# Kernel tuning notes

Hardware: AMD Instinct MI355X
Metric: run time of the kernel (lower is better)

## Reference

```python
import jax, jax.numpy as jnp
import numpy as np

N_NODES = 50000
N_EDGES = 600000
IN_DIM = 16
HIDDEN = 128
OUT_DIM = 4


def _sage_conv(x, src, dst, Wl, Wr, b, n_nodes):
    # PyG SAGEConv (aggr='mean'): out = lin_l(mean_{j in N(i)} x_j) + lin_r(x_i)
    msg = x[src]  # [E, F] gather
    s = jax.ops.segment_sum(msg, dst, num_segments=n_nodes)  # [N, F]
    cnt = jax.ops.segment_sum(jnp.ones((src.shape[0], 1), x.dtype), dst,
                              num_segments=n_nodes)  # [N, 1]
    agg = s / jnp.maximum(cnt, 1.0)
    return agg @ Wl.T + x @ Wr.T + b


def setup_inputs() -> dict:
    key = jax.random.key(0)
    ks = jax.random.split(key, 12)
    def glorot(k, shape):
        lim = np.sqrt(6.0 / (shape[0] + shape[1])).astype(np.float32)
        return jax.random.uniform(k, shape, jnp.float32, -lim, lim)
    x = jax.random.normal(ks[0], (N_NODES, IN_DIM), jnp.float32)
    edge_index = jax.random.randint(ks[1], (2, N_EDGES), 0, N_NODES, jnp.int64)
    return {
        "x": x,
        "edge_index": edge_index,
        "Wl1": glorot(ks[2], (HIDDEN, IN_DIM)),
        "Wr1": glorot(ks[3], (HIDDEN, IN_DIM)),
        "b1": jnp.zeros((HIDDEN,), jnp.float32),
        "Wl2": glorot(ks[4], (HIDDEN, HIDDEN)),
        "Wr2": glorot(ks[5], (HIDDEN, HIDDEN)),
        "b2": jnp.zeros((HIDDEN,), jnp.float32),
        "Wl3": glorot(ks[6], (HIDDEN, HIDDEN)),
        "Wr3": glorot(ks[7], (HIDDEN, HIDDEN)),
        "b3": jnp.zeros((HIDDEN,), jnp.float32),
        "Wh": glorot(ks[8], (OUT_DIM, HIDDEN)),
        "bh": jnp.zeros((OUT_DIM,), jnp.float32),
    }


def reference(x, edge_index, Wl1, Wr1, b1, Wl2, Wr2, b2, Wl3, Wr3, b3, Wh, bh):
    src, dst = edge_index[0], edge_index[1]
    n = x.shape[0]
    # dropout is identity in eval mode
    h = jax.nn.relu(_sage_conv(x, src, dst, Wl1, Wr1, b1, n))
    h = jax.nn.relu(_sage_conv(h, src, dst, Wl2, Wr2, b2, n))
    h = jax.nn.relu(_sage_conv(h, src, dst, Wl3, Wr3, b3, n))
    return h @ Wh.T + bh
```

## Files before the change

### kernel.cpp

```cpp
#include <hip/hip_runtime.h>
#include <hip/hip_bf16.h>


#define DEG_SLOTS 64

typedef unsigned short bf16_t;
typedef unsigned int uint32;
typedef __attribute__((ext_vector_type(8))) short bf16x8;
typedef __attribute__((ext_vector_type(4))) float f32x4;

__device__ __forceinline__ bf16_t f2bf(float f) {
    uint32 u = __float_as_uint(f);
    u += 0x7fff + ((u >> 16) & 1);
    return (bf16_t)(u >> 16);
}
__device__ __forceinline__ float bf2f(bf16_t b) {
    return __uint_as_float((uint32)b << 16);
}
__device__ __forceinline__ void acc8(float* acc, uint4 v) {
    acc[0] += bf2f((bf16_t)(v.x & 0xffff)); acc[1] += bf2f((bf16_t)(v.x >> 16));
    acc[2] += bf2f((bf16_t)(v.y & 0xffff)); acc[3] += bf2f((bf16_t)(v.y >> 16));
    acc[4] += bf2f((bf16_t)(v.z & 0xffff)); acc[5] += bf2f((bf16_t)(v.z >> 16));
    acc[6] += bf2f((bf16_t)(v.w & 0xffff)); acc[7] += bf2f((bf16_t)(v.w >> 16));
}

__global__ __launch_bounds__(256) void fill_padded_kernel(
    const int* __restrict__ src, const int* __restrict__ dst,
    int* __restrict__ cnt, int* __restrict__ colp, int E) {
    int i = blockIdx.x * 256 + threadIdx.x;
    int e0 = i * 4;
    if (e0 + 3 < E) {
        int4 s = *(const int4*)&src[e0];
        int4 d = *(const int4*)&dst[e0];
        int p0 = atomicAdd(&cnt[d.x], 1);
        int p1 = atomicAdd(&cnt[d.y], 1);
        int p2 = atomicAdd(&cnt[d.z], 1);
        int p3 = atomicAdd(&cnt[d.w], 1);
        if (p0 < DEG_SLOTS) colp[d.x * DEG_SLOTS + p0] = s.x;
        if (p1 < DEG_SLOTS) colp[d.y * DEG_SLOTS + p1] = s.y;
        if (p2 < DEG_SLOTS) colp[d.z * DEG_SLOTS + p2] = s.z;
        if (p3 < DEG_SLOTS) colp[d.w * DEG_SLOTS + p3] = s.w;
    } else {
        for (int e = e0; e < E; ++e) {
            int d = dst[e];
            int pos = atomicAdd(&cnt[d], 1);
            if (pos < DEG_SLOTS) colp[d * DEG_SLOTS + pos] = src[e];
        }
    }
}

__global__ __launch_bounds__(256) void layer16_fused_kernel(
    const float* __restrict__ x, const int* __restrict__ cnt,
    const int* __restrict__ colp,
    const float* __restrict__ Wl1, const float* __restrict__ Wr1,
    const float* __restrict__ bias, bf16_t* __restrict__ hout, int n) {
    const int t = threadIdx.x;
    const int lane = t & 63;
    const int wave = t >> 6;
    const int r = lane & 15;
    const int q = lane >> 4;
    const int qh = q & 1;
    const int qe = q >> 1;
    const int m0 = blockIdx.x * 32 + (wave >> 1) * 16;
    const int nb = (wave & 1) * 64;

    bf16x8 aF;
    {
        int node = m0 + r;
        if (node >= n) node = n - 1;
        float acc[8];
        #pragma unroll
        for (int j = 0; j < 8; ++j) acc[j] = 0.f;
        const int d = cnt[node];
        const int lo = node * DEG_SLOTS;
        const int hi = lo + d;
        int e = lo + qe;
        int c0 = 0, c1 = 0;
        if (e < hi) c0 = colp[e];
        if (e + 2 < hi) c1 = colp[e + 2];
        for (; e + 2 < hi; e += 4) {
            const int p0 = c0, p1 = c1;
            if (e + 4 < hi) c0 = colp[e + 4];
            if (e + 6 < hi) c1 = colp[e + 6];
            float4 u0 = *(const float4*)&x[p0 * 16 + qh * 8];
            float4 u1 = *(const float4*)&x[p0 * 16 + qh * 8 + 4];
            float4 u2 = *(const float4*)&x[p1 * 16 + qh * 8];
            float4 u3 = *(const float4*)&x[p1 * 16 + qh * 8 + 4];
            acc[0] += u0.x + u2.x; acc[1] += u0.y + u2.y;
            acc[2] += u0.z + u2.z; acc[3] += u0.w + u2.w;
            acc[4] += u1.x + u3.x; acc[5] += u1.y + u3.y;
            acc[6] += u1.z + u3.z; acc[7] += u1.w + u3.w;
        }
        if (e < hi) {
            float4 u0 = *(const float4*)&x[c0 * 16 + qh * 8];
            float4 u1 = *(const float4*)&x[c0 * 16 + qh * 8 + 4];
            acc[0] += u0.x; acc[1] += u0.y; acc[2] += u0.z; acc[3] += u0.w;
            acc[4] += u1.x; acc[5] += u1.y; acc[6] += u1.z; acc[7] += u1.w;
        }
        #pragma unroll
        for (int j = 0; j < 8; ++j) acc[j] += __shfl_xor(acc[j], 32);
        if (q < 2) {
            float iv = 1.0f / (float)max(d, 1);
            #pragma unroll
            for (int j = 0; j < 8; ++j) acc[j] *= iv;
        } else {
            float4 u0 = *(const float4*)&x[node * 16 + qh * 8];
            float4 u1 = *(const float4*)&x[node * 16 + qh * 8 + 4];
            acc[0] = u0.x; acc[1] = u0.y; acc[2] = u0.z; acc[3] = u0.w;
            acc[4] = u1.x; acc[5] = u1.y; acc[6] = u1.z; acc[7] = u1.w;
        }
        #pragma unroll
        for (int j = 0; j < 8; ++j) aF[j] = (short)f2bf(acc[j]);
    }

    #pragma unroll
    for (int nt = 0; nt < 4; ++nt) {
        const int cidx = nb + nt * 16 + r;
        const float* wsrc = (q < 2) ? (Wl1 + cidx * 16 + qh * 8)
                                    : (Wr1 + cidx * 16 + qh * 8);
        float4 w0 = *(const float4*)wsrc;
        float4 w1 = *(const float4*)(wsrc + 4);
        bf16x8 bF;
        bF[0] = (short)f2bf(w0.x); bF[1] = (short)f2bf(w0.y);
        bF[2] = (short)f2bf(w0.z); bF[3] = (short)f2bf(w0.w);
        bF[4] = (short)f2bf(w1.x); bF[5] = (short)f2bf(w1.y);
        bF[6] = (short)f2bf(w1.z); bF[7] = (short)f2bf(w1.w);
        f32x4 acc0 = {0.f, 0.f, 0.f, 0.f};
        acc0 = __builtin_amdgcn_mfma_f32_16x16x32_bf16(aF, bF, acc0, 0, 0, 0);
        float bo = bias[cidx];
        #pragma unroll
        for (int reg = 0; reg < 4; ++reg) {
            int row0 = m0 + q * 4 + reg;
            if (row0 < n)
                hout[(size_t)row0 * 128 + cidx] = f2bf(fmaxf(acc0[reg] + bo, 0.0f));
        }
    }
}

__global__ __launch_bounds__(256) void aggregate128_kernel(
    const bf16_t* __restrict__ h, const int* __restrict__ cnt,
    const int* __restrict__ colp,
    bf16_t* __restrict__ aggb, int N) {
    const int t = threadIdx.x;
    const int node = blockIdx.x * 8 + (t >> 5);
    const int sub = (t >> 4) & 1;
    const int li = t & 15;
    if (node >= N) return;
    const int d = cnt[node];
    const int lo = node * DEG_SLOTS;
    const int hi = lo + d;
    float acc[8];
    #pragma unroll
    for (int j = 0; j < 8; ++j) acc[j] = 0.0f;
    int e = lo + sub;
    int c0 = 0, c1 = 0, c2 = 0, c3 = 0;
    if (e < hi)     c0 = colp[e];
    if (e + 2 < hi) c1 = colp[e + 2];
    if (e + 4 < hi) c2 = colp[e + 4];
    if (e + 6 < hi) c3 = colp[e + 6];
    for (; e + 6 < hi; e += 8) {
        const int s0 = c0, s1 = c1, s2 = c2, s3 = c3;
        if (e + 8  < hi) c0 = colp[e + 8];
        if (e + 10 < hi) c1 = colp[e + 10];
        if (e + 12 < hi) c2 = colp[e + 12];
        if (e + 14 < hi) c3 = colp[e + 14];
        uint4 v0 = *(const uint4*)&h[(size_t)s0 * 128 + li * 8];
        uint4 v1 = *(const uint4*)&h[(size_t)s1 * 128 + li * 8];
        uint4 v2 = *(const uint4*)&h[(size_t)s2 * 128 + li * 8];
        uint4 v3 = *(const uint4*)&h[(size_t)s3 * 128 + li * 8];
        acc8(acc, v0);
        acc8(acc, v1);
        acc8(acc, v2);
        acc8(acc, v3);
    }
    if (e < hi) {
        uint4 v = *(const uint4*)&h[(size_t)c0 * 128 + li * 8];
        acc8(acc, v);
    }
    if (e + 2 < hi) {
        uint4 v = *(const uint4*)&h[(size_t)c1 * 128 + li * 8];
        acc8(acc, v);
    }
    if (e + 4 < hi) {
        uint4 v = *(const uint4*)&h[(size_t)c2 * 128 + li * 8];
        acc8(acc, v);
    }
    #pragma unroll
    for (int j = 0; j < 8; ++j) acc[j] += __shfl_xor(acc[j], 16);
    if (sub == 0) {
        const float iv = 1.0f / (float)max(d, 1);
        uint4 pk;
        pk.x = (uint32)f2bf(acc[0] * iv) | ((uint32)f2bf(acc[1] * iv) << 16);
        pk.y = (uint32)f2bf(acc[2] * iv) | ((uint32)f2bf(acc[3] * iv) << 16);
        pk.z = (uint32)f2bf(acc[4] * iv) | ((uint32)f2bf(acc[5] * iv) << 16);
        pk.w = (uint32)f2bf(acc[6] * iv) | ((uint32)f2bf(acc[7] * iv) << 16);
        *(uint4*)&aggb[(size_t)node * 128 + li * 8] = pk;
    }
}

__global__ __launch_bounds__(256) void layer128_mfma_kernel(
    const bf16_t* __restrict__ aggb, const bf16_t* __restrict__ hin,
    const float* __restrict__ Wl, const float* __restrict__ Wr,
    const float* __restrict__ bias, bf16_t* __restrict__ hout, int n) {
    __shared__ bf16_t w_lds[16384];

    const int t = threadIdx.x;
    const int lane = t & 63;
    const int wave = t >> 6;
    const int r = lane & 15;
    const int q = lane >> 4;
    const int c = blockIdx.x & 1;
    const int rowblk = blockIdx.x >> 1;
    const int nbase = c * 64;
    const int m0w = rowblk * 128 + wave * 32;

    #pragma unroll
    for (int i = 0; i < 8; ++i) {
        int ch  = i * 256 + t;
        int q_  = ch & 3;
        int r_  = (ch >> 2) & 15;
        int ks_ = (ch >> 6) & 7;
        int nt_ = ch >> 9;
        int cidx = nbase + nt_ * 16 + r_;
        int k0 = ks_ * 32 + q_ * 8;
        const float* src = (k0 < 128) ? (Wl + cidx * 128 + k0)
                                      : (Wr + cidx * 128 + (k0 - 128));
        float4 a = *(const float4*)src;
        float4 b = *(const float4*)(src + 4);
        uint4 pk;
        pk.x = (uint32)f2bf(a.x) | ((uint32)f2bf(a.y) << 16);
        pk.y = (uint32)f2bf(a.z) | ((uint32)f2bf(a.w) << 16);
        pk.z = (uint32)f2bf(b.x) | ((uint32)f2bf(b.y) << 16);
        pk.w = (uint32)f2bf(b.z) | ((uint32)f2bf(b.w) << 16);
        *(uint4*)&w_lds[ch * 8] = pk;
    }

    bf16x8 aF[2][8];
    #pragma unroll
    for (int mt = 0; mt < 2; ++mt) {
        int node = m0w + mt * 16 + r;
        if (node >= n) node = n - 1;
        const bf16_t* arow = aggb + (size_t)node * 128;
        const bf16_t* hrow = hin + (size_t)node * 128;
        #pragma unroll
        for (int ks = 0; ks < 4; ++ks)
            aF[mt][ks] = *(const bf16x8*)(arow + ks * 32 + q * 8);
        #pragma unroll
        for (int ks = 0; ks < 4; ++ks)
            aF[mt][4 + ks] = *(const bf16x8*)(hrow + ks * 32 + q * 8);
    }
    __syncthreads();

    #pragma unroll
    for (int nt = 0; nt < 4; ++nt) {
        f32x4 acc0 = {0.f, 0.f, 0.f, 0.f};
        f32x4 acc1 = {0.f, 0.f, 0.f, 0.f};
        #pragma unroll
        for (int ks = 0; ks < 8; ++ks) {
            bf16x8 bF = *(const bf16x8*)&w_lds[(size_t)((nt * 8 + ks) * 64 + r * 4 + q) * 8];
            acc0 = __builtin_amdgcn_mfma_f32_16x16x32_bf16(aF[0][ks], bF, acc0, 0, 0, 0);
            acc1 = __builtin_amdgcn_mfma_f32_16x16x32_bf16(aF[1][ks], bF, acc1, 0, 0, 0);
        }
        const int cidx = nbase + nt * 16 + r;
        const float bo = bias[cidx];
        #pragma unroll
        for (int reg = 0; reg < 4; ++reg) {
            int row0 = m0w + q * 4 + reg;
            if (row0 < n)
                hout[(size_t)row0 * 128 + cidx] = f2bf(fmaxf(acc0[reg] + bo, 0.0f));
            int row1 = m0w + 16 + q * 4 + reg;
            if (row1 < n)
                hout[(size_t)row1 * 128 + cidx] = f2bf(fmaxf(acc1[reg] + bo, 0.0f));
        }
    }
}

__global__ __launch_bounds__(256) void layer128_head_kernel(
    const bf16_t* __restrict__ aggb, const bf16_t* __restrict__ hin,
    const float* __restrict__ Wl, const float* __restrict__ Wr,
    const float* __restrict__ bias, const float* __restrict__ Wh,
    const float* __restrict__ bh, float* __restrict__ out, int n) {
    __shared__ bf16_t w_lds[16384];

    const int t = threadIdx.x;
    const int lane = t & 63;
    const int wave = t >> 6;
    const int r = lane & 15;
    const int q = lane >> 4;
    const int m0w = blockIdx.x * 64 + wave * 16;

    bf16x8 aF[8];
    {
        int node = m0w + r;
        if (node >= n) node = n - 1;
        const bf16_t* arow = aggb + (size_t)node * 128;
        const bf16_t* hrow = hin + (size_t)node * 128;
        #pragma unroll
        for (int ks = 0; ks < 4; ++ks)
            aF[ks] = *(const bf16x8*)(arow + ks * 32 + q * 8);
        #pragma unroll
        for (int ks = 0; ks < 4; ++ks)
            aF[4 + ks] = *(const bf16x8*)(hrow + ks * 32 + q * 8);
    }

    float p[4][4];
    #pragma unroll
    for (int reg = 0; reg < 4; ++reg)
        #pragma unroll
        for (int o = 0; o < 4; ++o) p[reg][o] = 0.f;

    #pragma unroll
    for (int phase = 0; phase < 2; ++phase) {
        if (phase) __syncthreads();
        const int nbase = phase * 64;
        #pragma unroll
        for (int i = 0; i < 8; ++i) {
            int ch  = i * 256 + t;
            int q_  = ch & 3;
            int r_  = (ch >> 2) & 15;
            int ks_ = (ch >> 6) & 7;
            int nt_ = ch >> 9;
            int cidx = nbase + nt_ * 16 + r_;
            int k0 = ks_ * 32 + q_ * 8;
            const float* src = (k0 < 128) ? (Wl + cidx * 128 + k0)
                                          : (Wr + cidx * 128 + (k0 - 128));
            float4 a = *(const float4*)src;
            float4 b = *(const float4*)(src + 4);
            uint4 pk;
            pk.x = (uint32)f2bf(a.x) | ((uint32)f2bf(a.y) << 16);
            pk.y = (uint32)f2bf(a.z) | ((uint32)f2bf(a.w) << 16);
            pk.z = (uint32)f2bf(b.x) | ((uint32)f2bf(b.y) << 16);
            pk.w = (uint32)f2bf(b.z) | ((uint32)f2bf(b.w) << 16);
            *(uint4*)&w_lds[ch * 8] = pk;
        }
        __syncthreads();

        #pragma unroll
        for (int nt = 0; nt < 4; ++nt) {
            f32x4 acc0 = {0.f, 0.f, 0.f, 0.f};
            #pragma unroll
            for (int ks = 0; ks < 8; ++ks) {
                bf16x8 bF = *(const bf16x8*)&w_lds[(size_t)((nt * 8 + ks) * 64 + r * 4 + q) * 8];
                acc0 = __builtin_amdgcn_mfma_f32_16x16x32_bf16(aF[ks], bF, acc0, 0, 0, 0);
            }
            const int cidx = nbase + nt * 16 + r;
            const float bo = bias[cidx];
            const float wh0 = Wh[cidx], wh1 = Wh[128 + cidx];
            const float wh2 = Wh[256 + cidx], wh3 = Wh[384 + cidx];
            #pragma unroll
            for (int reg = 0; reg < 4; ++reg) {
                float h0 = fmaxf(acc0[reg] + bo, 0.0f);
                p[reg][0] += h0 * wh0; p[reg][1] += h0 * wh1;
                p[reg][2] += h0 * wh2; p[reg][3] += h0 * wh3;
            }
        }
    }

    #pragma unroll
    for (int reg = 0; reg < 4; ++reg)
        #pragma unroll
        for (int o = 0; o < 4; ++o) {
            float v = p[reg][o];
            v += __shfl_xor(v, 1);
            v += __shfl_xor(v, 2);
            v += __shfl_xor(v, 4);
            v += __shfl_xor(v, 8);
            if (r == 0) {
                int row = m0w + q * 4 + reg;
                if (row < n) out[(size_t)row * 4 + o] = v + bh[o];
            }
        }
}

extern "C" void kernel_launch(void* const* d_in, const int* in_sizes, int n_in,
                              void* d_out, int out_size, void* d_ws, size_t ws_size,
                              hipStream_t stream) {
    const float* x   = (const float*)d_in[0];
    const int*   ei  = (const int*)d_in[1];
    const float* Wl1 = (const float*)d_in[2];
    const float* Wr1 = (const float*)d_in[3];
    const float* b1  = (const float*)d_in[4];
    const float* Wl2 = (const float*)d_in[5];
    const float* Wr2 = (const float*)d_in[6];
    const float* b2  = (const float*)d_in[7];
    const float* Wl3 = (const float*)d_in[8];
    const float* Wr3 = (const float*)d_in[9];
    const float* b3  = (const float*)d_in[10];
    const float* Wh  = (const float*)d_in[11];
    const float* bh  = (const float*)d_in[12];
    float* out = (float*)d_out;

    const int N = in_sizes[0] / 16;
    const int E = in_sizes[1] / 2;
    const int* src = ei;
    const int* dst = ei + E;

    int* cnt       = (int*)d_ws;
    int* colp      = cnt + ((N + 64) & ~63);
    bf16_t* aggb   = (bf16_t*)(colp + (size_t)N * DEG_SLOTS);
    bf16_t* hA     = aggb + (size_t)N * 128;
    bf16_t* hB     = hA + (size_t)N * 128;

    const int B = 256;
    auto blocks = [](long total, int b) { return (int)((total + b - 1) / b); };

    hipMemsetAsync(cnt, 0, (size_t)N * sizeof(int), stream);
    fill_padded_kernel<<<blocks((E + 3) / 4, B), B, 0, stream>>>(src, dst, cnt, colp, E);

    layer16_fused_kernel<<<blocks(N, 32), B, 0, stream>>>(
        x, cnt, colp, Wl1, Wr1, b1, hA, N);

    aggregate128_kernel<<<blocks(N, 8), B, 0, stream>>>(hA, cnt, colp, aggb, N);
    layer128_mfma_kernel<<<2 * blocks(N, 128), B, 0, stream>>>(
        aggb, hA, Wl2, Wr2, b2, hB, N);

    aggregate128_kernel<<<blocks(N, 8), B, 0, stream>>>(hB, cnt, colp, aggb, N);
    layer128_head_kernel<<<blocks(N, 64), B, 0, stream>>>(
        aggb, hB, Wl3, Wr3, b3, Wh, bh, out, N);
}
```

Baseline: 216.5 us.

## Fuse mean aggregation into layer-2 and layer-3 GEMM kernels

Removes the standalone aggregate128 launches. Each 64-node block of the GEMM kernel now first computes the neighbour means for its own rows, writing them to aggb, syncs, then reads them back for the MFMA GEMM. Layer 2 switches from 128-row x 64-col tiles to 64-row tiles covering all 128 columns in two weight phases, like the head kernel. This saves launches and keeps aggregates hot in cache, but serialises the gather latency with the GEMM inside each block and reloads weights per 64 rows.

After: 241.0 us. 1.11x slower.

```diff
diff --git a/kernel.cpp b/kernel.cpp
--- a/kernel.cpp
+++ b/kernel.cpp
@@ -137,12 +137,11 @@
     }
 }
 
-__global__ __launch_bounds__(256) void aggregate128_kernel(
-    const bf16_t* __restrict__ h, const int* __restrict__ cnt,
-    const int* __restrict__ colp,
-    bf16_t* __restrict__ aggb, int N) {
+__device__ __forceinline__ void aggregate8(
+    int nbase8, const bf16_t* __restrict__ h, const int* __restrict__ cnt,
+    const int* __restrict__ colp, bf16_t* __restrict__ aggb, int N) {
     const int t = threadIdx.x;
-    const int node = blockIdx.x * 8 + (t >> 5);
+    const int node = nbase8 + (t >> 5);
     const int sub = (t >> 4) & 1;
     const int li = t & 15;
     if (node >= N) return;
@@ -198,10 +197,12 @@
     }
 }
 
-__global__ __launch_bounds__(256) void layer128_mfma_kernel(
-    const bf16_t* __restrict__ aggb, const bf16_t* __restrict__ hin,
+__global__ __launch_bounds__(256) void fused_agg_gemm_kernel(
+    const bf16_t* __restrict__ hin, const int* __restrict__ cnt,
+    const int* __restrict__ colp,
     const float* __restrict__ Wl, const float* __restrict__ Wr,
-    const float* __restrict__ bias, bf16_t* __restrict__ hout, int n) {
+    const float* __restrict__ bias,
+    bf16_t* __restrict__ aggb, bf16_t* __restrict__ hout, int n) {
     __shared__ bf16_t w_lds[16384];
 
     const int t = threadIdx.x;
@@ -209,86 +210,14 @@
     const int wave = t >> 6;
     const int r = lane & 15;
     const int q = lane >> 4;
-    const int c = blockIdx.x & 1;
-    const int rowblk = blockIdx.x >> 1;
-    const int nbase = c * 64;
-    const int m0w = rowblk * 128 + wave * 32;
-
-    #pragma unroll
-    for (int i = 0; i < 8; ++i) {
-        int ch  = i * 256 + t;
-        int q_  = ch & 3;
-        int r_  = (ch >> 2) & 15;
-        int ks_ = (ch >> 6) & 7;
-        int nt_ = ch >> 9;
-        int cidx = nbase + nt_ * 16 + r_;
-        int k0 = ks_ * 32 + q_ * 8;
-        const float* src = (k0 < 128) ? (Wl + cidx * 128 + k0)
-                                      : (Wr + cidx * 128 + (k0 - 128));
-        float4 a = *(const float4*)src;
-        float4 b = *(const float4*)(src + 4);
-        uint4 pk;
-        pk.x = (uint32)f2bf(a.x) | ((uint32)f2bf(a.y) << 16);
-        pk.y = (uint32)f2bf(a.z) | ((uint32)f2bf(a.w) << 16);
-        pk.z = (uint32)f2bf(b.x) | ((uint32)f2bf(b.y) << 16);
-        pk.w = (uint32)f2bf(b.z) | ((uint32)f2bf(b.w) << 16);
-        *(uint4*)&w_lds[ch * 8] = pk;
-    }
-
-    bf16x8 aF[2][8];
-    #pragma unroll
-    for (int mt = 0; mt < 2; ++mt) {
-        int node = m0w + mt * 16 + r;
-        if (node >= n) node = n - 1;
-        const bf16_t* arow = aggb + (size_t)node * 128;
-        const bf16_t* hrow = hin + (size_t)node * 128;
-        #pragma unroll
-        for (int ks = 0; ks < 4; ++ks)
-            aF[mt][ks] = *(const bf16x8*)(arow + ks * 32 + q * 8);
-        #pragma unroll
-        for (int ks = 0; ks < 4; ++ks)
-            aF[mt][4 + ks] = *(const bf16x8*)(hrow + ks * 32 + q * 8);
-    }
+    const int nb0 = blockIdx.x * 64;
+
+    #pragma unroll
+    for (int i = 0; i < 8; ++i)
+        aggregate8(nb0 + i * 8, hin, cnt, colp, aggb, n);
     __syncthreads();
 
-    #pragma unroll
-    for (int nt = 0; nt < 4; ++nt) {
-        f32x4 acc0 = {0.f, 0.f, 0.f, 0.f};
-        f32x4 acc1 = {0.f, 0.f, 0.f, 0.f};
-        #pragma unroll
-        for (int ks = 0; ks < 8; ++ks) {
-            bf16x8 bF = *(const bf16x8*)&w_lds[(size_t)((nt * 8 + ks) * 64 + r * 4 + q) * 8];
-            acc0 = __builtin_amdgcn_mfma_f32_16x16x32_bf16(aF[0][ks], bF, acc0, 0, 0, 0);
-            acc1 = __builtin_amdgcn_mfma_f32_16x16x32_bf16(aF[1][ks], bF, acc1, 0, 0, 0);
-        }
-        const int cidx = nbase + nt * 16 + r;
-        const float bo = bias[cidx];
-        #pragma unroll
-        for (int reg = 0; reg < 4; ++reg) {
-            int row0 = m0w + q * 4 + reg;
-            if (row0 < n)
-                hout[(size_t)row0 * 128 + cidx] = f2bf(fmaxf(acc0[reg] + bo, 0.0f));
-            int row1 = m0w + 16 + q * 4 + reg;
-            if (row1 < n)
-                hout[(size_t)row1 * 128 + cidx] = f2bf(fmaxf(acc1[reg] + bo, 0.0f));
-        }
-    }
-}
-
-__global__ __launch_bounds__(256) void layer128_head_kernel(
-    const bf16_t* __restrict__ aggb, const bf16_t* __restrict__ hin,
-    const float* __restrict__ Wl, const float* __restrict__ Wr,
-    const float* __restrict__ bias, const float* __restrict__ Wh,
-    const float* __restrict__ bh, float* __restrict__ out, int n) {
-    __shared__ bf16_t w_lds[16384];
-
-    const int t = threadIdx.x;
-    const int lane = t & 63;
-    const int wave = t >> 6;
-    const int r = lane & 15;
-    const int q = lane >> 4;
-    const int m0w = blockIdx.x * 64 + wave * 16;
-
+    const int m0w = nb0 + wave * 16;
     bf16x8 aF[8];
     {
         int node = m0w + r;
@@ -302,12 +231,6 @@
         for (int ks = 0; ks < 4; ++ks)
             aF[4 + ks] = *(const bf16x8*)(hrow + ks * 32 + q * 8);
     }
-
-    float p[4][4];
-    #pragma unroll
-    for (int reg = 0; reg < 4; ++reg)
-        #pragma unroll
-        for (int o = 0; o < 4; ++o) p[reg][o] = 0.f;
 
     #pragma unroll
     for (int phase = 0; phase < 2; ++phase) {
@@ -345,6 +268,94 @@
             }
             const int cidx = nbase + nt * 16 + r;
             const float bo = bias[cidx];
+            #pragma unroll
+            for (int reg = 0; reg < 4; ++reg) {
+                int row = m0w + q * 4 + reg;
+                if (row < n)
+                    hout[(size_t)row * 128 + cidx] = f2bf(fmaxf(acc0[reg] + bo, 0.0f));
+            }
+        }
+    }
+}
+
+__global__ __launch_bounds__(256) void fused_agg_head_kernel(
+    const bf16_t* __restrict__ hin, const int* __restrict__ cnt,
+    const int* __restrict__ colp,
+    const float* __restrict__ Wl, const float* __restrict__ Wr,
+    const float* __restrict__ bias, const float* __restrict__ Wh,
+    const float* __restrict__ bh,
+    bf16_t* __restrict__ aggb, float* __restrict__ out, int n) {
+    __shared__ bf16_t w_lds[16384];
+
+    const int t = threadIdx.x;
+    const int lane = t & 63;
+    const int wave = t >> 6;
+    const int r = lane & 15;
+    const int q = lane >> 4;
+    const int nb0 = blockIdx.x * 64;
+
+    #pragma unroll
+    for (int i = 0; i < 8; ++i)
+        aggregate8(nb0 + i * 8, hin, cnt, colp, aggb, n);
+    __syncthreads();
+
+    const int m0w = nb0 + wave * 16;
+    bf16x8 aF[8];
+    {
+        int node = m0w + r;
+        if (node >= n) node = n - 1;
+        const bf16_t* arow = aggb + (size_t)node * 128;
+        const bf16_t* hrow = hin + (size_t)node * 128;
+        #pragma unroll
+        for (int ks = 0; ks < 4; ++ks)
+            aF[ks] = *(const bf16x8*)(arow + ks * 32 + q * 8);
+        #pragma unroll
+        for (int ks = 0; ks < 4; ++ks)
+            aF[4 + ks] = *(const bf16x8*)(hrow + ks * 32 + q * 8);
+    }
+
+    float p[4][4];
+    #pragma unroll
+    for (int reg = 0; reg < 4; ++reg)
+        #pragma unroll
+        for (int o = 0; o < 4; ++o) p[reg][o] = 0.f;
+
+    #pragma unroll
+    for (int phase = 0; phase < 2; ++phase) {
+        if (phase) __syncthreads();
+        const int nbase = phase * 64;
+        #pragma unroll
+        for (int i = 0; i < 8; ++i) {
+            int ch  = i * 256 + t;
+            int q_  = ch & 3;
+            int r_  = (ch >> 2) & 15;
+            int ks_ = (ch >> 6) & 7;
+            int nt_ = ch >> 9;
+            int cidx = nbase + nt_ * 16 + r_;
+            int k0 = ks_ * 32 + q_ * 8;
+            const float* src = (k0 < 128) ? (Wl + cidx * 128 + k0)
+                                          : (Wr + cidx * 128 + (k0 - 128));
+            float4 a = *(const float4*)src;
+            float4 b = *(const float4*)(src + 4);
+            uint4 pk;
+            pk.x = (uint32)f2bf(a.x) | ((uint32)f2bf(a.y) << 16);
+            pk.y = (uint32)f2bf(a.z) | ((uint32)f2bf(a.w) << 16);
+            pk.z = (uint32)f2bf(b.x) | ((uint32)f2bf(b.y) << 16);
+            pk.w = (uint32)f2bf(b.z) | ((uint32)f2bf(b.w) << 16);
+            *(uint4*)&w_lds[ch * 8] = pk;
+        }
+        __syncthreads();
+
+        #pragma unroll
+        for (int nt = 0; nt < 4; ++nt) {
+            f32x4 acc0 = {0.f, 0.f, 0.f, 0.f};
+            #pragma unroll
+            for (int ks = 0; ks < 8; ++ks) {
+                bf16x8 bF = *(const bf16x8*)&w_lds[(size_t)((nt * 8 + ks) * 64 + r * 4 + q) * 8];
+                acc0 = __builtin_amdgcn_mfma_f32_16x16x32_bf16(aF[ks], bF, acc0, 0, 0, 0);
+            }
+            const int cidx = nbase + nt * 16 + r;
+            const float bo = bias[cidx];
             const float wh0 = Wh[cidx], wh1 = Wh[128 + cidx];
             const float wh2 = Wh[256 + cidx], wh3 = Wh[384 + cidx];
             #pragma unroll
@@ -410,11 +421,9 @@
     layer16_fused_kernel<<<blocks(N, 32), B, 0, stream>>>(
         x, cnt, colp, Wl1, Wr1, b1, hA, N);
 
-    aggregate128_kernel<<<blocks(N, 8), B, 0, stream>>>(hA, cnt, colp, aggb, N);
-    layer128_mfma_kernel<<<2 * blocks(N, 128), B, 0, stream>>>(
-        aggb, hA, Wl2, Wr2, b2, hB, N);
-
-    aggregate128_kernel<<<blocks(N, 8), B, 0, stream>>>(hB, cnt, colp, aggb, N);
-    layer128_head_kernel<<<blocks(N, 64), B, 0, stream>>>(
-        aggb, hB, Wl3, Wr3, b3, Wh, bh, out, N);
-}
+    fused_agg_gemm_kernel<<<blocks(N, 64), B, 0, stream>>>(
+        hA, cnt, colp, Wl2, Wr2, b2, aggb, hB, N);
+
+    fused_agg_head_kernel<<<blocks(N, 64), B, 0, stream>>>(
+        hB, cnt, colp, Wl3, Wr3, b3, Wh, bh, aggb, out, N);
+}
```
